# Optimization experiments

Measured on AMD Instinct MI355X. Metric: run time of the kernel, lower is better.

## Reference

```python
import jax, jax.numpy as jnp
import numpy as np

N, NFEAT, NHID, NCLASS, H1 = 4096, 512, 64, 16, 8
GAIN = 1.414  # xavier gain used by the torch module
NEG_SLOPE = 0.2
MASK_VAL = -1e10


def _xavier(k, shape):
    fan_in, fan_out = shape[-2], shape[-1]
    lim = GAIN * (6.0 / (fan_in + fan_out)) ** 0.5
    return jax.random.uniform(k, shape, jnp.float32, -lim, lim)


def setup_inputs() -> dict:
    key = jax.random.key(0)
    ks = jax.random.split(key, 10)
    return {
        "x": jax.random.normal(ks[0], (N, NFEAT), jnp.float32),
        "adj": jax.random.randint(ks[1], (N, N), 0, 2, jnp.int32),
        # layer-1 parameters, stacked over H1 heads
        "W1": _xavier(ks[2], (H1, NFEAT, NHID)),
        "b1": jnp.zeros((H1, NHID), jnp.float32),
        "as1": _xavier(ks[3], (H1, NHID, 1))[..., 0],
        "an1": _xavier(ks[4], (H1, NHID, 1))[..., 0],
        # layer-2 parameters (single head, input = H1*NHID due to concat)
        "W2": _xavier(ks[5], (H1 * NHID, NCLASS)),
        "b2": jnp.zeros((NCLASS,), jnp.float32),
        "as2": _xavier(ks[6], (NCLASS, 1))[:, 0],
        "an2": _xavier(ks[7], (NCLASS, 1))[:, 0],
    }


def gat_layer(X, adj_pos, W, b, a_s, a_n):
    # X: [N, Fin], W: [Fin, Fout], a_s/a_n: [Fout], adj_pos: [N, N] bool
    feats = X @ W                                        # [N, Fout]
    s = feats @ a_s                                      # [N]
    nb = feats @ a_n                                     # [N]
    attn = jax.nn.leaky_relu(s[:, None] + nb[None, :], NEG_SLOPE)  # [N, N]
    attn = jnp.where(adj_pos, attn, MASK_VAL)
    attn = jax.nn.softmax(attn, axis=-1)
    # dropout on attn/feats is a no-op in eval mode
    return attn @ feats + b                              # [N, Fout]


def reference(x, adj, W1, b1, as1, an1, W2, b2, as2, an2):
    adj_pos = adj > 0
    # x dropout is a no-op in eval mode
    layer1 = jax.vmap(gat_layer, in_axes=(None, None, 0, 0, 0, 0))
    h = jax.nn.relu(layer1(x, adj_pos, W1, b1, as1, an1))    # [H1, N, NHID]
    h = jnp.transpose(h, (1, 0, 2)).reshape(N, H1 * NHID)    # concat heads on dim 1
    h = jax.nn.elu(h)
    out = jax.nn.relu(gat_layer(h, adj_pos, W2, b2, as2, an2))  # [N, NCLASS]
    return jax.nn.log_softmax(out, axis=1)
```

## Files before the change

kernel.cpp:

```cpp
#include <hip/hip_runtime.h>

#define NN 4096
#define NFEAT 512
#define NHID 64
#define H1 8
#define NCLS 16
#define BND 40.0f
#define VSTR 72

typedef short bf16x8 __attribute__((ext_vector_type(8)));
typedef float f32x4 __attribute__((ext_vector_type(4)));

__device__ __forceinline__ unsigned short f2bf(float f) {
    unsigned u = __float_as_uint(f);
    u += 0x7fffu + ((u >> 16) & 1u);
    return (unsigned short)(u >> 16);
}
__device__ __forceinline__ float leaky(float v) { return fmaxf(v, 0.2f * v); }
__device__ __forceinline__ unsigned pkbf(float lo, float hi) {
    return __builtin_amdgcn_perm(__float_as_uint(hi) + 0x8000u,
                                 __float_as_uint(lo) + 0x8000u, 0x07060302u);
}
__device__ __forceinline__ bf16x8 mk8(unsigned a, unsigned b, unsigned c, unsigned d) {
    union { unsigned u[4]; bf16x8 v; } cv;
    cv.u[0] = a; cv.u[1] = b; cv.u[2] = c; cv.u[3] = d; return cv.v;
}

__global__ __launch_bounds__(256)
void k_prep(const int* __restrict__ adj, unsigned long long* __restrict__ bits,
            const float* __restrict__ W1, unsigned short* __restrict__ W1bT)
{
    __shared__ float wt[64][65];
    const int t = threadIdx.x, bx = blockIdx.x;
    if (bx < NN) {
        const int wv = t >> 6, lane = t & 63;
        const int* ap = adj + (size_t)bx * NN;
        for (int w = wv; w < 64; w += 4) {
            unsigned long long m = __ballot(ap[w * 64 + lane] > 0);
            if (lane == 0) bits[(size_t)bx * 64 + w] = m;
        }
        return;
    }
    const int kt = (bx - NN) & 7, h = (bx - NN) >> 3;
    #pragma unroll
    for (int i = 0; i < 4; ++i) {
        const int f = t + 256 * i;
        const int r = f >> 4, c4 = f & 15;
        const float4 v = *(const float4*)(W1 + ((size_t)(h * NFEAT) + kt * 64 + r) * NHID + c4 * 4);
        wt[r][c4 * 4 + 0] = v.x; wt[r][c4 * 4 + 1] = v.y;
        wt[r][c4 * 4 + 2] = v.z; wt[r][c4 * 4 + 3] = v.w;
    }
    __syncthreads();
    const int c = t >> 2, kq = t & 3;
    #pragma unroll
    for (int i = 0; i < 4; ++i) {
        const int k = kq * 16 + i * 4;
        uint2 w;
        w.x = (unsigned)f2bf(wt[k + 0][c]) | ((unsigned)f2bf(wt[k + 1][c]) << 16);
        w.y = (unsigned)f2bf(wt[k + 2][c]) | ((unsigned)f2bf(wt[k + 3][c]) << 16);
        *(uint2*)(W1bT + ((size_t)h * NHID + c) * NFEAT + kt * 64 + k) = w;
    }
}

__global__ __launch_bounds__(256)
void k_feats1(const float* __restrict__ x, const unsigned short* __restrict__ W1bT,
              const float* __restrict__ as1, const float* __restrict__ an1,
              unsigned short* __restrict__ f1bT, float* __restrict__ s1,
              float* __restrict__ F1a, float* __restrict__ F2a)
{
    const int t = threadIdx.x, wv = t >> 6, lane = t & 63;
    const int q = lane >> 4, n = lane & 15;
    const int h = blockIdx.y, R0 = blockIdx.x * 64;
    const int row = R0 + wv * 16 + n;
    const float* ap = x + (size_t)row * NFEAT;
    const unsigned short* wp = W1bT + (size_t)h * NHID * NFEAT;
    f32x4 acc[4] = {{0.f,0.f,0.f,0.f},{0.f,0.f,0.f,0.f},{0.f,0.f,0.f,0.f},{0.f,0.f,0.f,0.f}};
    #pragma unroll 4
    for (int k0 = 0; k0 < NFEAT; k0 += 32) {
        const float4 xa = *(const float4*)(ap + k0 + q * 8);
        const float4 xb = *(const float4*)(ap + k0 + q * 8 + 4);
        const bf16x8 af = mk8(pkbf(xa.x, xa.y), pkbf(xa.z, xa.w),
                              pkbf(xb.x, xb.y), pkbf(xb.z, xb.w));
        #pragma unroll
        for (int nt = 0; nt < 4; ++nt) {
            const bf16x8 bf = *(const bf16x8*)(wp + (size_t)(nt * 16 + n) * NFEAT + k0 + q * 8);
            acc[nt] = __builtin_amdgcn_mfma_f32_16x16x32_bf16(af, bf, acc[nt], 0, 0, 0);
        }
    }
    #pragma unroll
    for (int nt = 0; nt < 4; ++nt) {
        uint2 w;
        w.x = (unsigned)f2bf(acc[nt][0]) | ((unsigned)f2bf(acc[nt][1]) << 16);
        w.y = (unsigned)f2bf(acc[nt][2]) | ((unsigned)f2bf(acc[nt][3]) << 16);
        *(uint2*)(f1bT + ((size_t)h * NHID + nt * 16 + n) * NN + R0 + wv * 16 + q * 4) = w;
    }
    float asv[4], anv[4];
    #pragma unroll
    for (int nt = 0; nt < 4; ++nt) {
        asv[nt] = as1[h * NHID + nt * 16 + n];
        anv[nt] = an1[h * NHID + nt * 16 + n];
    }
    #pragma unroll
    for (int i = 0; i < 4; ++i) {
        float ps = acc[0][i]*asv[0] + acc[1][i]*asv[1] + acc[2][i]*asv[2] + acc[3][i]*asv[3];
        float pn = acc[0][i]*anv[0] + acc[1][i]*anv[1] + acc[2][i]*anv[2] + acc[3][i]*anv[3];
        #pragma unroll
        for (int off = 8; off > 0; off >>= 1) {
            ps += __shfl_xor(ps, off, 64);
            pn += __shfl_xor(pn, off, 64);
        }
        if (n == 0) {
            const int idx = R0 + wv * 16 + q * 4 + i;
            s1[h * NN + idx] = ps;
            F1a[h * NN + idx] = __expf(pn - BND);
            F2a[h * NN + idx] = __expf(0.2f * (pn - BND));
        }
    }
}

__global__ __launch_bounds__(256)
void k_gat1(const unsigned short* __restrict__ f1bT, const float* __restrict__ s1,
            const float* __restrict__ F1, const float* __restrict__ F2,
            const unsigned long long* __restrict__ abits, const float* __restrict__ b1,
            unsigned short* __restrict__ hcatb)
{
    __shared__ __align__(16) char smem[4 * 64 * VSTR * 2];
    unsigned short* vT = (unsigned short*)smem;

    const int t = threadIdx.x, wv = t >> 6, lane = t & 63;
    const int q = lane >> 4, n = lane & 15;
    const int rg = wv >> 1, jh = wv & 1;
    const int h = blockIdx.y, R0 = blockIdx.x * 32;
    const int row = R0 + rg * 16 + n;
    const float v = s1[h * NN + row] + BND;
    const float mhat = leaky(v);
    const float E1 = __expf(v - mhat), E2 = __expf(0.2f * v - mhat);
    const unsigned long long* arow = abits + (size_t)row * 64;
    const float* F1p = F1 + (size_t)h * NN;
    const float* F2p = F2 + (size_t)h * NN;

    const unsigned short* sbase = f1bT + (size_t)h * NHID * NN + (size_t)(t >> 3) * NN + (t & 7) * 8;
    const int dof = (t >> 3) * VSTR + (t & 7) * 8;

    f32x4 acc[4] = {{0.f,0.f,0.f,0.f},{0.f,0.f,0.f,0.f},{0.f,0.f,0.f,0.f},{0.f,0.f,0.f,0.f}};
    float lsum = 0.f;

    {
        int4 a0 = *(const int4*)(sbase + 0);
        int4 a1 = *(const int4*)(sbase + (size_t)32 * NN + 0);
        int4 b0 = *(const int4*)(sbase + 2048);
        int4 b1v = *(const int4*)(sbase + (size_t)32 * NN + 2048);
        *(int4*)(vT + 0 * (64 * VSTR) + dof) = a0;
        *(int4*)(vT + 0 * (64 * VSTR) + dof + 32 * VSTR) = a1;
        *(int4*)(vT + 2 * (64 * VSTR) + dof) = b0;
        *(int4*)(vT + 2 * (64 * VSTR) + dof + 32 * VSTR) = b1v;
    }
    __syncthreads();

    for (int it = 0; it < 32; ++it) {
        const int db = it & 1;
        int4 na0, na1, nb0, nb1v;
        if (it < 31) {
            const int jn = (it + 1) * 64;
            na0  = *(const int4*)(sbase + jn);
            na1  = *(const int4*)(sbase + (size_t)32 * NN + jn);
            nb0  = *(const int4*)(sbase + 2048 + jn);
            nb1v = *(const int4*)(sbase + (size_t)32 * NN + 2048 + jn);
        }
        const int j0 = jh * 2048 + it * 64;
        const unsigned long long a64 = arow[j0 >> 6];
        const unsigned short* tbase = vT + (jh * 2 + db) * (64 * VSTR);
        #pragma unroll
        for (int ch = 0; ch < 2; ++ch) {
            const int kb = ch * 32 + q * 8;
            const float4 f1a = *(const float4*)(F1p + j0 + kb);
            const float4 f1b = *(const float4*)(F1p + j0 + kb + 4);
            const float4 f2a = *(const float4*)(F2p + j0 + kb);
            const float4 f2b = *(const float4*)(F2p + j0 + kb + 4);
            const float F1v[8] = {f1a.x, f1a.y, f1a.z, f1a.w, f1b.x, f1b.y, f1b.z, f1b.w};
            const float F2v[8] = {f2a.x, f2a.y, f2a.z, f2a.w, f2b.x, f2b.y, f2b.z, f2b.w};
            const unsigned b8 = (unsigned)(a64 >> kb) & 0xffu;
            unsigned au[4];
            #pragma unroll
            for (int jp = 0; jp < 4; ++jp) {
                float p0 = fmaxf(E1 * F1v[2*jp],   E2 * F2v[2*jp]);
                float p1 = fmaxf(E1 * F1v[2*jp+1], E2 * F2v[2*jp+1]);
                p0 = ((b8 >> (2*jp)) & 1u) ? p0 : 0.f;
                p1 = ((b8 >> (2*jp+1)) & 1u) ? p1 : 0.f;
                lsum += p0 + p1;
                au[jp] = pkbf(p0, p1);
            }
            const bf16x8 af = mk8(au[0], au[1], au[2], au[3]);
            #pragma unroll
            for (int nt = 0; nt < 4; ++nt) {
                const bf16x8 bf = *(const bf16x8*)(tbase + (nt * 16 + n) * VSTR + kb);
                acc[nt] = __builtin_amdgcn_mfma_f32_16x16x32_bf16(af, bf, acc[nt], 0, 0, 0);
            }
        }
        if (it < 31) {
            const int dbn = db ^ 1;
            *(int4*)(vT + (0 * 2 + dbn) * (64 * VSTR) + dof) = na0;
            *(int4*)(vT + (0 * 2 + dbn) * (64 * VSTR) + dof + 32 * VSTR) = na1;
            *(int4*)(vT + (1 * 2 + dbn) * (64 * VSTR) + dof) = nb0;
            *(int4*)(vT + (1 * 2 + dbn) * (64 * VSTR) + dof + 32 * VSTR) = nb1v;
        }
        __syncthreads();
    }

    lsum += __shfl_xor(lsum, 16, 64);
    lsum += __shfl_xor(lsum, 32, 64);

    float* cmbf = (float*)smem;
    float* lwf  = (float*)(smem + 17408);
    #pragma unroll
    for (int nt = 0; nt < 4; ++nt)
        #pragma unroll
        for (int i = 0; i < 4; ++i)
            cmbf[(jh * 32 + rg * 16 + q * 4 + i) * 68 + nt * 16 + n] = acc[nt][i];
    if (q == 0) lwf[jh * 32 + rg * 16 + n] = lsum;
    __syncthreads();

    const int col = t & 63, rgrp = t >> 6;
    const float bv = b1[h * NHID + col];
    #pragma unroll
    for (int rr = 0; rr < 8; ++rr) {
        const int r = rgrp * 8 + rr;
        const float tot = cmbf[r * 68 + col] + cmbf[(32 + r) * 68 + col];
        const float lt  = lwf[r] + lwf[32 + r];
        hcatb[(size_t)(R0 + r) * (H1 * NHID) + h * NHID + col] =
            f2bf(fmaxf(tot / lt + bv, 0.f));
    }
}

__global__ __launch_bounds__(128)
void k_feats2(const unsigned short* __restrict__ hcatb, const float* __restrict__ W2,
              const float* __restrict__ as2, const float* __restrict__ an2,
              unsigned short* __restrict__ f2bT, float* __restrict__ s2,
              float* __restrict__ F1b, float* __restrict__ F2b)
{
    __shared__ __align__(16) unsigned short w2T[NCLS][520];
    const int t = threadIdx.x, wv = t >> 6, lane = t & 63;
    const int q = lane >> 4, n = lane & 15;
    #pragma unroll
    for (int i = 0; i < 16; ++i) {
        const int f4 = t + 128 * i;
        const float4 v = ((const float4*)W2)[f4];
        const int k = f4 >> 2, c0 = (f4 & 3) * 4;
        w2T[c0 + 0][k] = f2bf(v.x); w2T[c0 + 1][k] = f2bf(v.y);
        w2T[c0 + 2][k] = f2bf(v.z); w2T[c0 + 3][k] = f2bf(v.w);
    }
    __syncthreads();

    const int R0 = blockIdx.x * 32;
    const int row = R0 + wv * 16 + n;
    const unsigned short* ap = hcatb + (size_t)row * NFEAT;
    f32x4 acc = {0.f, 0.f, 0.f, 0.f};
    #pragma unroll 4
    for (int k0 = 0; k0 < NFEAT; k0 += 32) {
        const bf16x8 af = *(const bf16x8*)(ap + k0 + q * 8);
        const bf16x8 bf = *(const bf16x8*)&w2T[n][k0 + q * 8];
        acc = __builtin_amdgcn_mfma_f32_16x16x32_bf16(af, bf, acc, 0, 0, 0);
    }
    uint2 w;
    w.x = (unsigned)f2bf(acc[0]) | ((unsigned)f2bf(acc[1]) << 16);
    w.y = (unsigned)f2bf(acc[2]) | ((unsigned)f2bf(acc[3]) << 16);
    *(uint2*)(f2bT + (size_t)n * NN + R0 + wv * 16 + q * 4) = w;
    const float asv = as2[n], anv = an2[n];
    #pragma unroll
    for (int i = 0; i < 4; ++i) {
        float ps = acc[i] * asv, pn = acc[i] * anv;
        #pragma unroll
        for (int off = 8; off > 0; off >>= 1) {
            ps += __shfl_xor(ps, off, 64);
            pn += __shfl_xor(pn, off, 64);
        }
        if (n == 0) {
            const int idx = R0 + wv * 16 + q * 4 + i;
            s2[idx] = ps;
            F1b[idx] = __expf(pn - BND);
            F2b[idx] = __expf(0.2f * (pn - BND));
        }
    }
}

__global__ __launch_bounds__(512)
void k_gat2(const unsigned short* __restrict__ f2bT, const float* __restrict__ s2,
            const float* __restrict__ F1, const float* __restrict__ F2,
            const unsigned long long* __restrict__ abits, const float* __restrict__ b2,
            float* __restrict__ out)
{
    __shared__ float cmb[8][16][17];
    __shared__ float lw[8][16];
    const int t = threadIdx.x, wv = t >> 6, lane = t & 63;
    const int q = lane >> 4, n = lane & 15;
    const int R0 = blockIdx.x * 16, row = R0 + n;
    const float v = s2[row] + BND, mhat = leaky(v);
    const float E1 = __expf(v - mhat), E2 = __expf(0.2f * v - mhat);
    const unsigned long long* arow = abits + (size_t)row * 64;

    f32x4 acc = {0.f, 0.f, 0.f, 0.f};
    float lsum = 0.f;
    const int jbeg = wv * 512;
    for (int j0 = jbeg; j0 < jbeg + 512; j0 += 64) {
        const unsigned long long a64 = arow[j0 >> 6];
        #pragma unroll
        for (int ch = 0; ch < 2; ++ch) {
            const int kb = ch * 32 + q * 8;
            const float4 f1a = *(const float4*)(F1 + j0 + kb);
            const float4 f1b = *(const float4*)(F1 + j0 + kb + 4);
            const float4 f2a = *(const float4*)(F2 + j0 + kb);
            const float4 f2b = *(const float4*)(F2 + j0 + kb + 4);
            const float F1v[8] = {f1a.x, f1a.y, f1a.z, f1a.w, f1b.x, f1b.y, f1b.z, f1b.w};
            const float F2v[8] = {f2a.x, f2a.y, f2a.z, f2a.w, f2b.x, f2b.y, f2b.z, f2b.w};
            const unsigned b8 = (unsigned)(a64 >> kb) & 0xffu;
            unsigned au[4];
            #pragma unroll
            for (int jp = 0; jp < 4; ++jp) {
                float p0 = fmaxf(E1 * F1v[2*jp],   E2 * F2v[2*jp]);
                float p1 = fmaxf(E1 * F1v[2*jp+1], E2 * F2v[2*jp+1]);
                p0 = ((b8 >> (2*jp)) & 1u) ? p0 : 0.f;
                p1 = ((b8 >> (2*jp+1)) & 1u) ? p1 : 0.f;
                lsum += p0 + p1;
                au[jp] = pkbf(p0, p1);
            }
            const bf16x8 af = mk8(au[0], au[1], au[2], au[3]);
            const bf16x8 bf = *(const bf16x8*)(f2bT + (size_t)n * NN + j0 + kb);
            acc = __builtin_amdgcn_mfma_f32_16x16x32_bf16(af, bf, acc, 0, 0, 0);
        }
    }
    lsum += __shfl_xor(lsum, 16, 64);
    lsum += __shfl_xor(lsum, 32, 64);
    #pragma unroll
    for (int i = 0; i < 4; ++i) cmb[wv][q * 4 + i][n] = acc[i];
    if (q == 0) lw[wv][n] = lsum;
    __syncthreads();

    if (t < 256) {
        const int r = t >> 4, c = t & 15;
        float tot = 0.f, lt = 0.f;
        #pragma unroll
        for (int w8 = 0; w8 < 8; ++w8) { tot += cmb[w8][r][c]; lt += lw[w8][r]; }
        float val = fmaxf(tot / lt + b2[c], 0.f);
        float mx = val;
        #pragma unroll
        for (int off = 1; off < 16; off <<= 1) mx = fmaxf(mx, __shfl_xor(mx, off, 64));
        const float e = __expf(val - mx);
        float se = e;
        #pragma unroll
        for (int off = 1; off < 16; off <<= 1) se += __shfl_xor(se, off, 64);
        out[(size_t)(R0 + r) * NCLS + c] = val - mx - __logf(se);
    }
}

extern "C" void kernel_launch(void* const* d_in, const int* in_sizes, int n_in,
                              void* d_out, int out_size, void* d_ws, size_t ws_size,
                              hipStream_t stream)
{
    const float* x   = (const float*)d_in[0];
    const int*   adj = (const int*)  d_in[1];
    const float* W1  = (const float*)d_in[2];
    const float* b1  = (const float*)d_in[3];
    const float* as1 = (const float*)d_in[4];
    const float* an1 = (const float*)d_in[5];
    const float* W2  = (const float*)d_in[6];
    const float* b2  = (const float*)d_in[7];
    const float* as2 = (const float*)d_in[8];
    const float* an2 = (const float*)d_in[9];
    float* out = (float*)d_out;

    char* ws = (char*)d_ws;
    unsigned long long* abits = (unsigned long long*)(ws);
    unsigned short* f1bT  = (unsigned short*)(ws + (2u << 20));
    unsigned short* hcatb = (unsigned short*)(ws + (6u << 20));
    unsigned short* W1bT  = (unsigned short*)(ws + (10u << 20));
    char* ws2 = ws + (10u << 20) + (512u << 10);
    float* s1   = (float*)(ws2);
    float* F1a  = (float*)(ws2 + (128u << 10));
    float* F2a  = (float*)(ws2 + (256u << 10));
    unsigned short* f2bT = (unsigned short*)(ws2 + (384u << 10));
    float* s2   = (float*)(ws2 + (512u << 10));
    float* F1b  = (float*)(ws2 + (528u << 10));
    float* F2b  = (float*)(ws2 + (544u << 10));

    k_prep  <<<dim3(NN + 64),     256, 0, stream>>>(adj, abits, W1, W1bT);
    k_feats1<<<dim3(NN / 64, H1), 256, 0, stream>>>(x, W1bT, as1, an1, f1bT, s1, F1a, F2a);
    k_gat1  <<<dim3(NN / 32, H1), 256, 0, stream>>>(f1bT, s1, F1a, F2a, abits, b1, hcatb);
    k_feats2<<<dim3(NN / 32),     128, 0, stream>>>(hcatb, W2, as2, an2, f2bT, s2, F1b, F2b);
    k_gat2  <<<dim3(NN / 16),     512, 0, stream>>>(f2bT, s2, F1b, F2b, abits, b2, out);
}
```

Measured before the change: 234.7 us.

## Retile GAT layer-1 attention for 64-row blocks and pre-swizzle W1 fragments

The layer-1 attention kernel now uses 512-thread blocks covering 64 rows. Each wave computes two 16-row groups that share every LDS value fragment, and the neighbour range is split four ways. This halves staging traffic per output row but doubles accumulator registers and grows LDS to about 73 KB. W1 is also pre-packed into MFMA fragment order so k_feats1 reads its B operand contiguously. In addition, bf16 packing switches to the perm-based helper (round-half-up, where the old one rounded to nearest even), and k_gat2 doubles its waves per block with a shorter j-range each.

```diff
diff --git a/kernel.cpp b/kernel.cpp
--- a/kernel.cpp
+++ b/kernel.cpp
@@ -28,7 +28,7 @@
 
 __global__ __launch_bounds__(256)
 void k_prep(const int* __restrict__ adj, unsigned long long* __restrict__ bits,
-            const float* __restrict__ W1, unsigned short* __restrict__ W1bT)
+            const float* __restrict__ W1, unsigned short* __restrict__ w1f)
 {
     __shared__ float wt[64][65];
     const int t = threadIdx.x, bx = blockIdx.x;
@@ -51,19 +51,25 @@
         wt[r][c4 * 4 + 2] = v.z; wt[r][c4 * 4 + 3] = v.w;
     }
     __syncthreads();
-    const int c = t >> 2, kq = t & 3;
-    #pragma unroll
-    for (int i = 0; i < 4; ++i) {
-        const int k = kq * 16 + i * 4;
-        uint2 w;
-        w.x = (unsigned)f2bf(wt[k + 0][c]) | ((unsigned)f2bf(wt[k + 1][c]) << 16);
-        w.y = (unsigned)f2bf(wt[k + 2][c]) | ((unsigned)f2bf(wt[k + 3][c]) << 16);
-        *(uint2*)(W1bT + ((size_t)h * NHID + c) * NFEAT + kt * 64 + k) = w;
+    #pragma unroll
+    for (int s = 0; s < 2; ++s) {
+        const int o = t + s * 256;
+        const int kg2 = o >> 8, rem = o & 255;
+        const int nt = rem >> 6, lane2 = rem & 63;
+        const int qq = lane2 >> 4, nn = lane2 & 15;
+        const int kl = kg2 * 32 + qq * 8;
+        const int c = nt * 16 + nn;
+        uint4 w;
+        w.x = pkbf(wt[kl + 0][c], wt[kl + 1][c]);
+        w.y = pkbf(wt[kl + 2][c], wt[kl + 3][c]);
+        w.z = pkbf(wt[kl + 4][c], wt[kl + 5][c]);
+        w.w = pkbf(wt[kl + 6][c], wt[kl + 7][c]);
+        *(uint4*)(w1f + (((size_t)h * 16 + kt * 2 + kg2) * 4 + nt) * 512 + lane2 * 8) = w;
     }
 }
 
 __global__ __launch_bounds__(256)
-void k_feats1(const float* __restrict__ x, const unsigned short* __restrict__ W1bT,
+void k_feats1(const float* __restrict__ x, const unsigned short* __restrict__ w1f,
               const float* __restrict__ as1, const float* __restrict__ an1,
               unsigned short* __restrict__ f1bT, float* __restrict__ s1,
               float* __restrict__ F1a, float* __restrict__ F2a)
@@ -73,25 +79,25 @@
     const int h = blockIdx.y, R0 = blockIdx.x * 64;
     const int row = R0 + wv * 16 + n;
     const float* ap = x + (size_t)row * NFEAT;
-    const unsigned short* wp = W1bT + (size_t)h * NHID * NFEAT;
+    const unsigned short* wp = w1f + (size_t)h * 16 * 4 * 512 + lane * 8;
     f32x4 acc[4] = {{0.f,0.f,0.f,0.f},{0.f,0.f,0.f,0.f},{0.f,0.f,0.f,0.f},{0.f,0.f,0.f,0.f}};
     #pragma unroll 4
-    for (int k0 = 0; k0 < NFEAT; k0 += 32) {
-        const float4 xa = *(const float4*)(ap + k0 + q * 8);
-        const float4 xb = *(const float4*)(ap + k0 + q * 8 + 4);
+    for (int kg = 0; kg < 16; ++kg) {
+        const float4 xa = *(const float4*)(ap + kg * 32 + q * 8);
+        const float4 xb = *(const float4*)(ap + kg * 32 + q * 8 + 4);
         const bf16x8 af = mk8(pkbf(xa.x, xa.y), pkbf(xa.z, xa.w),
                               pkbf(xb.x, xb.y), pkbf(xb.z, xb.w));
         #pragma unroll
         for (int nt = 0; nt < 4; ++nt) {
-            const bf16x8 bf = *(const bf16x8*)(wp + (size_t)(nt * 16 + n) * NFEAT + k0 + q * 8);
+            const bf16x8 bf = *(const bf16x8*)(wp + (size_t)(kg * 4 + nt) * 512);
             acc[nt] = __builtin_amdgcn_mfma_f32_16x16x32_bf16(af, bf, acc[nt], 0, 0, 0);
         }
     }
     #pragma unroll
     for (int nt = 0; nt < 4; ++nt) {
         uint2 w;
-        w.x = (unsigned)f2bf(acc[nt][0]) | ((unsigned)f2bf(acc[nt][1]) << 16);
-        w.y = (unsigned)f2bf(acc[nt][2]) | ((unsigned)f2bf(acc[nt][3]) << 16);
+        w.x = pkbf(acc[nt][0], acc[nt][1]);
+        w.y = pkbf(acc[nt][2], acc[nt][3]);
         *(uint2*)(f1bT + ((size_t)h * NHID + nt * 16 + n) * NN + R0 + wv * 16 + q * 4) = w;
     }
     float asv[4], anv[4];
@@ -118,58 +124,67 @@
     }
 }
 
-__global__ __launch_bounds__(256)
+__global__ __launch_bounds__(512, 4)
 void k_gat1(const unsigned short* __restrict__ f1bT, const float* __restrict__ s1,
             const float* __restrict__ F1, const float* __restrict__ F2,
             const unsigned long long* __restrict__ abits, const float* __restrict__ b1,
             unsigned short* __restrict__ hcatb)
 {
-    __shared__ __align__(16) char smem[4 * 64 * VSTR * 2];
+    __shared__ __align__(16) char smem[4 * 2 * 64 * VSTR * 2];
     unsigned short* vT = (unsigned short*)smem;
 
     const int t = threadIdx.x, wv = t >> 6, lane = t & 63;
     const int q = lane >> 4, n = lane & 15;
-    const int rg = wv >> 1, jh = wv & 1;
-    const int h = blockIdx.y, R0 = blockIdx.x * 32;
-    const int row = R0 + rg * 16 + n;
-    const float v = s1[h * NN + row] + BND;
-    const float mhat = leaky(v);
-    const float E1 = __expf(v - mhat), E2 = __expf(0.2f * v - mhat);
-    const unsigned long long* arow = abits + (size_t)row * 64;
+    const int rg = wv >> 2, jq = wv & 3;
+    const int h = blockIdx.y, R0 = blockIdx.x * 64;
+    const int rowA = R0 + rg * 32 + n;
+    const int rowB = rowA + 16;
+    const float vA = s1[h * NN + rowA] + BND, mhA = leaky(vA);
+    const float vB = s1[h * NN + rowB] + BND, mhB = leaky(vB);
+    const float E1A = __expf(vA - mhA), E2A = __expf(0.2f * vA - mhA);
+    const float E1B = __expf(vB - mhB), E2B = __expf(0.2f * vB - mhB);
+    const unsigned long long* arowA = abits + (size_t)rowA * 64;
+    const unsigned long long* arowB = abits + (size_t)rowB * 64;
     const float* F1p = F1 + (size_t)h * NN;
     const float* F2p = F2 + (size_t)h * NN;
 
-    const unsigned short* sbase = f1bT + (size_t)h * NHID * NN + (size_t)(t >> 3) * NN + (t & 7) * 8;
-    const int dof = (t >> 3) * VSTR + (t & 7) * 8;
-
-    f32x4 acc[4] = {{0.f,0.f,0.f,0.f},{0.f,0.f,0.f,0.f},{0.f,0.f,0.f,0.f},{0.f,0.f,0.f,0.f}};
-    float lsum = 0.f;
+    const int stile = t >> 7;
+    const int sc0 = (t & 127) >> 3, sj8 = t & 7;
+    const unsigned short* sbase = f1bT + (size_t)h * NHID * NN + (size_t)sc0 * NN + sj8 * 8;
+    const int dof = sc0 * VSTR + sj8 * 8;
+
+    f32x4 accA[4] = {{0.f,0.f,0.f,0.f},{0.f,0.f,0.f,0.f},{0.f,0.f,0.f,0.f},{0.f,0.f,0.f,0.f}};
+    f32x4 accB[4] = {{0.f,0.f,0.f,0.f},{0.f,0.f,0.f,0.f},{0.f,0.f,0.f,0.f},{0.f,0.f,0.f,0.f}};
+    float lsA = 0.f, lsB = 0.f;
 
     {
-        int4 a0 = *(const int4*)(sbase + 0);
-        int4 a1 = *(const int4*)(sbase + (size_t)32 * NN + 0);
-        int4 b0 = *(const int4*)(sbase + 2048);
-        int4 b1v = *(const int4*)(sbase + (size_t)32 * NN + 2048);
-        *(int4*)(vT + 0 * (64 * VSTR) + dof) = a0;
-        *(int4*)(vT + 0 * (64 * VSTR) + dof + 32 * VSTR) = a1;
-        *(int4*)(vT + 2 * (64 * VSTR) + dof) = b0;
-        *(int4*)(vT + 2 * (64 * VSTR) + dof + 32 * VSTR) = b1v;
+        const int js = stile * 1024;
+        int4 v0 = *(const int4*)(sbase + js);
+        int4 v1 = *(const int4*)(sbase + (size_t)16 * NN + js);
+        int4 v2 = *(const int4*)(sbase + (size_t)32 * NN + js);
+        int4 v3 = *(const int4*)(sbase + (size_t)48 * NN + js);
+        unsigned short* d = vT + (stile * 2 + 0) * (64 * VSTR) + dof;
+        *(int4*)(d) = v0;
+        *(int4*)(d + 16 * VSTR) = v1;
+        *(int4*)(d + 32 * VSTR) = v2;
+        *(int4*)(d + 48 * VSTR) = v3;
     }
     __syncthreads();
 
-    for (int it = 0; it < 32; ++it) {
+    for (int it = 0; it < 16; ++it) {
         const int db = it & 1;
-        int4 na0, na1, nb0, nb1v;
-        if (it < 31) {
-            const int jn = (it + 1) * 64;
-            na0  = *(const int4*)(sbase + jn);
-            na1  = *(const int4*)(sbase + (size_t)32 * NN + jn);
-            nb0  = *(const int4*)(sbase + 2048 + jn);
-            nb1v = *(const int4*)(sbase + (size_t)32 * NN + 2048 + jn);
-        }
-        const int j0 = jh * 2048 + it * 64;
-        const unsigned long long a64 = arow[j0 >> 6];
-        const unsigned short* tbase = vT + (jh * 2 + db) * (64 * VSTR);
+        int4 p0, p1, p2, p3;
+        if (it < 15) {
+            const int js = stile * 1024 + (it + 1) * 64;
+            p0 = *(const int4*)(sbase + js);
+            p1 = *(const int4*)(sbase + (size_t)16 * NN + js);
+            p2 = *(const int4*)(sbase + (size_t)32 * NN + js);
+            p3 = *(const int4*)(sbase + (size_t)48 * NN + js);
+        }
+        const int j0 = jq * 1024 + it * 64;
+        const unsigned long long aA = arowA[j0 >> 6];
+        const unsigned long long aB = arowB[j0 >> 6];
+        const unsigned short* tbase = vT + (jq * 2 + db) * (64 * VSTR);
         #pragma unroll
         for (int ch = 0; ch < 2; ++ch) {
             const int kb = ch * 32 + q * 8;
@@ -179,54 +194,72 @@
             const float4 f2b = *(const float4*)(F2p + j0 + kb + 4);
             const float F1v[8] = {f1a.x, f1a.y, f1a.z, f1a.w, f1b.x, f1b.y, f1b.z, f1b.w};
             const float F2v[8] = {f2a.x, f2a.y, f2a.z, f2a.w, f2b.x, f2b.y, f2b.z, f2b.w};
-            const unsigned b8 = (unsigned)(a64 >> kb) & 0xffu;
-            unsigned au[4];
+            const unsigned bA = (unsigned)(aA >> kb) & 0xffu;
+            const unsigned bB = (unsigned)(aB >> kb) & 0xffu;
+            unsigned uA[4], uB[4];
             #pragma unroll
             for (int jp = 0; jp < 4; ++jp) {
-                float p0 = fmaxf(E1 * F1v[2*jp],   E2 * F2v[2*jp]);
-                float p1 = fmaxf(E1 * F1v[2*jp+1], E2 * F2v[2*jp+1]);
-                p0 = ((b8 >> (2*jp)) & 1u) ? p0 : 0.f;
-                p1 = ((b8 >> (2*jp+1)) & 1u) ? p1 : 0.f;
-                lsum += p0 + p1;
-                au[jp] = pkbf(p0, p1);
+                float a0 = fmaxf(E1A * F1v[2*jp],   E2A * F2v[2*jp]);
+                float a1 = fmaxf(E1A * F1v[2*jp+1], E2A * F2v[2*jp+1]);
+                a0 = ((bA >> (2*jp)) & 1u) ? a0 : 0.f;
+                a1 = ((bA >> (2*jp+1)) & 1u) ? a1 : 0.f;
+                lsA += a0 + a1;
+                uA[jp] = pkbf(a0, a1);
+                float b0 = fmaxf(E1B * F1v[2*jp],   E2B * F2v[2*jp]);
+                float b1v = fmaxf(E1B * F1v[2*jp+1], E2B * F2v[2*jp+1]);
+                b0 = ((bB >> (2*jp)) & 1u) ? b0 : 0.f;
+                b1v = ((bB >> (2*jp+1)) & 1u) ? b1v : 0.f;
+                lsB += b0 + b1v;
+                uB[jp] = pkbf(b0, b1v);
             }
-            const bf16x8 af = mk8(au[0], au[1], au[2], au[3]);
+            const bf16x8 afA = mk8(uA[0], uA[1], uA[2], uA[3]);
+            const bf16x8 afB = mk8(uB[0], uB[1], uB[2], uB[3]);
             #pragma unroll
             for (int nt = 0; nt < 4; ++nt) {
                 const bf16x8 bf = *(const bf16x8*)(tbase + (nt * 16 + n) * VSTR + kb);
-                acc[nt] = __builtin_amdgcn_mfma_f32_16x16x32_bf16(af, bf, acc[nt], 0, 0, 0);
+                accA[nt] = __builtin_amdgcn_mfma_f32_16x16x32_bf16(afA, bf, accA[nt], 0, 0, 0);
+                accB[nt] = __builtin_amdgcn_mfma_f32_16x16x32_bf16(afB, bf, accB[nt], 0, 0, 0);
             }
         }
-        if (it < 31) {
-            const int dbn = db ^ 1;
-            *(int4*)(vT + (0 * 2 + dbn) * (64 * VSTR) + dof) = na0;
-            *(int4*)(vT + (0 * 2 + dbn) * (64 * VSTR) + dof + 32 * VSTR) = na1;
-            *(int4*)(vT + (1 * 2 + dbn) * (64 * VSTR) + dof) = nb0;
-            *(int4*)(vT + (1 * 2 + dbn) * (64 * VSTR) + dof + 32 * VSTR) = nb1v;
+        if (it < 15) {
+            unsigned short* d = vT + (stile * 2 + (db ^ 1)) * (64 * VSTR) + dof;
+            *(int4*)(d) = p0;
+            *(int4*)(d + 16 * VSTR) = p1;
+            *(int4*)(d + 32 * VSTR) = p2;
+            *(int4*)(d + 48 * VSTR) = p3;
         }
         __syncthreads();
     }
 
-    lsum += __shfl_xor(lsum, 16, 64);
-    lsum += __shfl_xor(lsum, 32, 64);
+    lsA += __shfl_xor(lsA, 16, 64); lsA += __shfl_xor(lsA, 32, 64);
+    lsB += __shfl_xor(lsB, 16, 64); lsB += __shfl_xor(lsB, 32, 64);
 
     float* cmbf = (float*)smem;
-    float* lwf  = (float*)(smem + 17408);
+    float* lwf  = (float*)(smem + 69632);
     #pragma unroll
     for (int nt = 0; nt < 4; ++nt)
         #pragma unroll
-        for (int i = 0; i < 4; ++i)
-            cmbf[(jh * 32 + rg * 16 + q * 4 + i) * 68 + nt * 16 + n] = acc[nt][i];
-    if (q == 0) lwf[jh * 32 + rg * 16 + n] = lsum;
+        for (int i = 0; i < 4; ++i) {
+            cmbf[((size_t)jq * 64 + rg * 32 + q * 4 + i) * 68 + nt * 16 + n] = accA[nt][i];
+            cmbf[((size_t)jq * 64 + rg * 32 + 16 + q * 4 + i) * 68 + nt * 16 + n] = accB[nt][i];
+        }
+    if (q == 0) {
+        lwf[jq * 64 + rg * 32 + n] = lsA;
+        lwf[jq * 64 + rg * 32 + 16 + n] = lsB;
+    }
     __syncthreads();
 
-    const int col = t & 63, rgrp = t >> 6;
+    const int col = t & 63, r8 = t >> 6;
     const float bv = b1[h * NHID + col];
     #pragma unroll
     for (int rr = 0; rr < 8; ++rr) {
-        const int r = rgrp * 8 + rr;
-        const float tot = cmbf[r * 68 + col] + cmbf[(32 + r) * 68 + col];
-        const float lt  = lwf[r] + lwf[32 + r];
+        const int r = r8 * 8 + rr;
+        float tot = 0.f, lt = 0.f;
+        #pragma unroll
+        for (int jj = 0; jj < 4; ++jj) {
+            tot += cmbf[((size_t)jj * 64 + r) * 68 + col];
+            lt  += lwf[jj * 64 + r];
+        }
         hcatb[(size_t)(R0 + r) * (H1 * NHID) + h * NHID + col] =
             f2bf(fmaxf(tot / lt + bv, 0.f));
     }
@@ -262,8 +295,8 @@
         acc = __builtin_amdgcn_mfma_f32_16x16x32_bf16(af, bf, acc, 0, 0, 0);
     }
     uint2 w;
-    w.x = (unsigned)f2bf(acc[0]) | ((unsigned)f2bf(acc[1]) << 16);
-    w.y = (unsigned)f2bf(acc[2]) | ((unsigned)f2bf(acc[3]) << 16);
+    w.x = pkbf(acc[0], acc[1]);
+    w.y = pkbf(acc[2], acc[3]);
     *(uint2*)(f2bT + (size_t)n * NN + R0 + wv * 16 + q * 4) = w;
     const float asv = as2[n], anv = an2[n];
     #pragma unroll
@@ -283,14 +316,14 @@
     }
 }
 
-__global__ __launch_bounds__(512)
+__global__ __launch_bounds__(1024)
 void k_gat2(const unsigned short* __restrict__ f2bT, const float* __restrict__ s2,
             const float* __restrict__ F1, const float* __restrict__ F2,
             const unsigned long long* __restrict__ abits, const float* __restrict__ b2,
             float* __restrict__ out)
 {
-    __shared__ float cmb[8][16][17];
-    __shared__ float lw[8][16];
+    __shared__ float cmb[16][16][17];
+    __shared__ float lw[16][16];
     const int t = threadIdx.x, wv = t >> 6, lane = t & 63;
     const int q = lane >> 4, n = lane & 15;
     const int R0 = blockIdx.x * 16, row = R0 + n;
@@ -300,8 +333,8 @@
 
     f32x4 acc = {0.f, 0.f, 0.f, 0.f};
     float lsum = 0.f;
-    const int jbeg = wv * 512;
-    for (int j0 = jbeg; j0 < jbeg + 512; j0 += 64) {
+    const int jbeg = wv * 256;
+    for (int j0 = jbeg; j0 < jbeg + 256; j0 += 64) {
         const unsigned long long a64 = arow[j0 >> 6];
         #pragma unroll
         for (int ch = 0; ch < 2; ++ch) {
@@ -339,7 +372,7 @@
         const int r = t >> 4, c = t & 15;
         float tot = 0.f, lt = 0.f;
         #pragma unroll
-        for (int w8 = 0; w8 < 8; ++w8) { tot += cmb[w8][r][c]; lt += lw[w8][r]; }
+        for (int w16 = 0; w16 < 16; ++w16) { tot += cmb[w16][r][c]; lt += lw[w16][r]; }
         float val = fmaxf(tot / lt + b2[c], 0.f);
         float mx = val;
         #pragma unroll
@@ -372,7 +405,7 @@
     unsigned long long* abits = (unsigned long long*)(ws);
     unsigned short* f1bT  = (unsigned short*)(ws + (2u << 20));
     unsigned short* hcatb = (unsigned short*)(ws + (6u << 20));
-    unsigned short* W1bT  = (unsigned short*)(ws + (10u << 20));
+    unsigned short* w1f   = (unsigned short*)(ws + (10u << 20));
     char* ws2 = ws + (10u << 20) + (512u << 10);
     float* s1   = (float*)(ws2);
     float* F1a  = (float*)(ws2 + (128u << 10));
@@ -382,9 +415,9 @@
     float* F1b  = (float*)(ws2 + (528u << 10));
     float* F2b  = (float*)(ws2 + (544u << 10));
 
-    k_prep  <<<dim3(NN + 64),     256, 0, stream>>>(adj, abits, W1, W1bT);
-    k_feats1<<<dim3(NN / 64, H1), 256, 0, stream>>>(x, W1bT, as1, an1, f1bT, s1, F1a, F2a);
-    k_gat1  <<<dim3(NN / 32, H1), 256, 0, stream>>>(f1bT, s1, F1a, F2a, abits, b1, hcatb);
+    k_prep  <<<dim3(NN + 64),     256, 0, stream>>>(adj, abits, W1, w1f);
+    k_feats1<<<dim3(NN / 64, H1), 256, 0, stream>>>(x, w1f, as1, an1, f1bT, s1, F1a, F2a);
+    k_gat1  <<<dim3(NN / 64, H1), 512, 0, stream>>>(f1bT, s1, F1a, F2a, abits, b1, hcatb);
     k_feats2<<<dim3(NN / 32),     128, 0, stream>>>(hcatb, W2, as2, an2, f2bT, s2, F1b, F2b);
-    k_gat2  <<<dim3(NN / 16),     512, 0, stream>>>(f2bT, s2, F1b, F2b, abits, b2, out);
-}
+    k_gat2  <<<dim3(NN / 16),     1024, 0, stream>>>(f2bT, s2, F1b, F2b, abits, b2, out);
+}
```

Result: faster. 209.8 us (-10.6%).
